# Optimization experiments

Measured on AMD Instinct MI355X. Metric: run time of the kernel, lower is better.

Reference implementation:

```python
import jax, jax.numpy as jnp
import numpy as np

N = 100000      # num nodes
E = 1600000     # num edges (avg degree 16)
IN = 128        # input_dim
D = 32          # output_dim per head
H = 4           # heads
ALPHA = 0.2     # LeakyReLU slope


def setup_inputs() -> dict:
    key = jax.random.key(0)
    k1, k2, k3, k4, k5 = jax.random.split(key, 5)
    X = jax.random.normal(k1, (N, IN), dtype=jnp.float32)
    # fc weights, xavier-like scale (bias=False in the module)
    W0 = jax.random.normal(k2, (H * D, IN), dtype=jnp.float32) * (1.0 / np.sqrt(IN))
    W1 = jax.random.normal(k3, (H * D, IN), dtype=jnp.float32) * (1.0 / np.sqrt(IN))
    a0 = jax.random.normal(k4, (H, 1, D), dtype=jnp.float32) * (1.0 / np.sqrt(D))
    deg = E // N
    # CSR rows expanded to sorted segment ids: every node has exactly `deg` out-edges
    edge_src = jnp.repeat(jnp.arange(N, dtype=jnp.int32), deg)
    column_index = jax.random.randint(k5, (E,), 0, N, dtype=jnp.int32)
    return {"X": X, "W0": W0, "W1": W1, "a0": a0,
            "edge_src": edge_src, "column_index": column_index}


def _leaky_relu(x):
    return jnp.where(x > 0, x, ALPHA * x)


def reference(X, W0, W1, a0, edge_src, column_index):
    # Linear projections, split per head: [H, N, D]
    X0 = _leaky_relu(X @ W0.T).reshape(N, H, D).transpose(1, 0, 2)
    X1 = _leaky_relu(X @ W1.T).reshape(N, H, D).transpose(1, 0, 2)
    a = a0[:, 0, :]                                    # [H, D]
    # SDDMM: att[h,e] = a[h] . (X0[h,src(e)] + X1[h,dst(e)])
    s0 = jnp.einsum('hnd,hd->hn', X0, a)               # [H, N]
    s1 = jnp.einsum('hnd,hd->hn', X1, a)
    att = s0[:, edge_src] + s1[:, column_index]        # [H, E]
    # per-head global min-max normalization, then exp (module's softmax surrogate)
    mx = jnp.max(att, axis=1, keepdims=True)
    mn = jnp.min(att, axis=1, keepdims=True)
    att = jnp.exp((att - mn) / (mx - mn))
    # sparse row-sum (softmax denominator): [N, H]
    rows_sum = jax.ops.segment_sum(att.T, edge_src, num_segments=N)
    # SpMM: aggregate neighbor features weighted by att -> [N, H, D]
    msg = att.T[:, :, None] * X1[:, column_index, :].transpose(1, 0, 2)  # [E, H, D]
    h_prime = jax.ops.segment_sum(msg, edge_src, num_segments=N)
    return h_prime / rows_sum[:, :, None]
```

## Files before the change

### kernel.cpp

```cpp
#include <hip/hip_runtime.h>
#include <hip/hip_bf16.h>

#define NN 100000
#define EE 1600000
#define ALPHA 0.2f
#define MM_BLOCKS 1563

typedef __bf16 bf16_t;
typedef __bf16 bf16x8 __attribute__((ext_vector_type(8)));
typedef __bf16 bf16x4 __attribute__((ext_vector_type(4)));
typedef float fx4 __attribute__((ext_vector_type(4)));


__global__ __launch_bounds__(512) void gemm_kernel(
    const float* __restrict__ X, const float* __restrict__ W0,
    const float* __restrict__ W1, const float* __restrict__ a0,
    bf16_t* __restrict__ F1, float* __restrict__ s0g, float* __restrict__ s1g)
{
  __shared__ uint4 lw[4096];
  const int tid  = threadIdx.x;
  const int wv   = tid >> 6;
  const int lane = tid & 63;
  const int col  = lane & 15;
  const int quad = lane >> 4;

#pragma unroll
  for (int i = 0; i < 8; ++i) {
    const int task = i * 512 + tid;
    const int sct = task >> 8, sks = (task >> 6) & 3, sl = task & 63;
    const int r  = sct * 16 + (sl & 15);
    const int c0 = (sks * 4 + (sl >> 4)) * 8;
    const float* src = (r < 128 ? W0 + (size_t)r * 128 : W1 + (size_t)(r - 128) * 128) + c0;
    const fx4 wa = *(const fx4*)src;
    const fx4 wb_ = *(const fx4*)(src + 4);
    bf16x8 wf;
    wf[0] = (bf16_t)wa[0]; wf[1] = (bf16_t)wa[1];
    wf[2] = (bf16_t)wa[2]; wf[3] = (bf16_t)wa[3];
    wf[4] = (bf16_t)wb_[0]; wf[5] = (bf16_t)wb_[1];
    wf[6] = (bf16_t)wb_[2]; wf[7] = (bf16_t)wb_[3];
    lw[task] = __builtin_bit_cast(uint4, wf);
  }
  __syncthreads();

  const int tile = blockIdx.x * 8 + wv;
  if (tile >= (NN / 16)) return;
  const int n0   = tile * 16;
  const int node = n0 + col;

  fx4 acc[16];
#pragma unroll
  for (int c = 0; c < 16; ++c) {
    acc[c][0] = 0.f; acc[c][1] = 0.f; acc[c][2] = 0.f; acc[c][3] = 0.f;
  }

  const float* xrow = X + (size_t)node * 128 + quad * 8;
#pragma unroll
  for (int ks = 0; ks < 4; ++ks) {
    fx4 xa = *(const fx4*)(xrow + ks * 32);
    fx4 xb = *(const fx4*)(xrow + ks * 32 + 4);
    bf16x8 xf;
    xf[0] = (bf16_t)xa[0]; xf[1] = (bf16_t)xa[1];
    xf[2] = (bf16_t)xa[2]; xf[3] = (bf16_t)xa[3];
    xf[4] = (bf16_t)xb[0]; xf[5] = (bf16_t)xb[1];
    xf[6] = (bf16_t)xb[2]; xf[7] = (bf16_t)xb[3];
#pragma unroll
    for (int ct = 0; ct < 16; ++ct) {
      const uint4 w4 = lw[(ct * 4 + ks) * 64 + lane];
      const bf16x8 wf = __builtin_bit_cast(bf16x8, w4);
      acc[ct] = __builtin_amdgcn_mfma_f32_16x16x32_bf16(wf, xf, acc[ct], 0, 0, 0);
    }
  }

  float sdot[8];
#pragma unroll
  for (int s = 0; s < 8; ++s) sdot[s] = 0.f;

#pragma unroll
  for (int ct = 0; ct < 16; ++ct) {
    const fx4 av = *(const fx4*)(a0 + (ct & 7) * 16 + quad * 4);
#pragma unroll
    for (int r = 0; r < 4; ++r) {
      float v = acc[ct][r];
      v = v > 0.f ? v : ALPHA * v;
      acc[ct][r] = v;
      sdot[ct >> 1] += v * av[r];
    }
    if (ct >= 8) {
      bf16x4 p;
      p[0] = (bf16_t)acc[ct][0]; p[1] = (bf16_t)acc[ct][1];
      p[2] = (bf16_t)acc[ct][2]; p[3] = (bf16_t)acc[ct][3];
      *(bf16x4*)(F1 + (size_t)node * 128 + (ct - 8) * 16 + quad * 4) = p;
    }
  }

#pragma unroll
  for (int s = 0; s < 8; ++s) {
    sdot[s] += __shfl_xor(sdot[s], 16);
    sdot[s] += __shfl_xor(sdot[s], 32);
  }
  if (quad == 0) {
    fx4 r0, r1;
    r0[0] = sdot[0]; r0[1] = sdot[1]; r0[2] = sdot[2]; r0[3] = sdot[3];
    r1[0] = sdot[4]; r1[1] = sdot[5]; r1[2] = sdot[6]; r1[3] = sdot[7];
    *(fx4*)(s0g + (size_t)node * 4) = r0;
    *(fx4*)(s1g + (size_t)node * 4) = r1;
  }
}

__global__ __launch_bounds__(256) void minmax1_kernel(
    const int* __restrict__ cidx, const float* __restrict__ s0g,
    const float* __restrict__ s1g, float* __restrict__ partial)
{
  __shared__ float s_red[4][8];
  const int t = blockIdx.x * 256 + threadIdx.x;
  fx4 mx, mn;
#pragma unroll
  for (int h = 0; h < 4; ++h) { mx[h] = -1e30f; mn[h] = 1e30f; }
  if (t < EE / 4) {
    const int node = t >> 2;
    const fx4 s0v = *(const fx4*)(s0g + (size_t)node * 4);
    const int4 c4 = ((const int4*)cidx)[t];
    const int cc[4] = {c4.x, c4.y, c4.z, c4.w};
#pragma unroll
    for (int j = 0; j < 4; ++j) {
      const fx4 s1v = *(const fx4*)(s1g + (size_t)cc[j] * 4);
#pragma unroll
      for (int h = 0; h < 4; ++h) {
        const float att = s0v[h] + s1v[h];
        mx[h] = fmaxf(mx[h], att);
        mn[h] = fminf(mn[h], att);
      }
    }
  }
#pragma unroll
  for (int off = 1; off < 64; off <<= 1) {
#pragma unroll
    for (int h = 0; h < 4; ++h) {
      mx[h] = fmaxf(mx[h], __shfl_xor(mx[h], off));
      mn[h] = fminf(mn[h], __shfl_xor(mn[h], off));
    }
  }
  const int wv = threadIdx.x >> 6;
  if ((threadIdx.x & 63) == 0) {
#pragma unroll
    for (int h = 0; h < 4; ++h) {
      s_red[wv][h] = mx[h];
      s_red[wv][4 + h] = mn[h];
    }
  }
  __syncthreads();
  if (threadIdx.x < 8) {
    const int s = threadIdx.x;
    float v = s_red[0][s];
    if (s < 4) { v = fmaxf(v, s_red[1][s]); v = fmaxf(v, s_red[2][s]); v = fmaxf(v, s_red[3][s]); }
    else       { v = fminf(v, s_red[1][s]); v = fminf(v, s_red[2][s]); v = fminf(v, s_red[3][s]); }
    partial[blockIdx.x * 8 + s] = v;
  }
}

__global__ __launch_bounds__(256) void minmax2_kernel(
    const float* __restrict__ partial, float* __restrict__ mm)
{
  __shared__ float s_red[4][8];
  fx4 mx, mn;
#pragma unroll
  for (int h = 0; h < 4; ++h) { mx[h] = -1e30f; mn[h] = 1e30f; }
  for (int g = threadIdx.x; g < MM_BLOCKS; g += 256) {
    const fx4 p0 = *(const fx4*)(partial + g * 8);
    const fx4 p1 = *(const fx4*)(partial + g * 8 + 4);
#pragma unroll
    for (int h = 0; h < 4; ++h) {
      mx[h] = fmaxf(mx[h], p0[h]);
      mn[h] = fminf(mn[h], p1[h]);
    }
  }
#pragma unroll
  for (int off = 1; off < 64; off <<= 1) {
#pragma unroll
    for (int h = 0; h < 4; ++h) {
      mx[h] = fmaxf(mx[h], __shfl_xor(mx[h], off));
      mn[h] = fminf(mn[h], __shfl_xor(mn[h], off));
    }
  }
  const int wv = threadIdx.x >> 6;
  if ((threadIdx.x & 63) == 0) {
#pragma unroll
    for (int h = 0; h < 4; ++h) {
      s_red[wv][h] = mx[h];
      s_red[wv][4 + h] = mn[h];
    }
  }
  __syncthreads();
  if (threadIdx.x < 8) {
    const int s = threadIdx.x;
    float v = s_red[0][s];
    if (s < 4) { v = fmaxf(v, s_red[1][s]); v = fmaxf(v, s_red[2][s]); v = fmaxf(v, s_red[3][s]); }
    else       { v = fminf(v, s_red[1][s]); v = fminf(v, s_red[2][s]); v = fminf(v, s_red[3][s]); }
    mm[s] = v;
  }
}

__global__ __launch_bounds__(256) void aggregate_kernel(
    const int* __restrict__ cidx, const float* __restrict__ s0g,
    const float* __restrict__ s1g, const bf16_t* __restrict__ F1,
    const float* __restrict__ mm, float* __restrict__ out)
{
  const int t = blockIdx.x * 256 + threadIdx.x;
  const int node = t >> 4;
  if (node >= NN) return;
  const int sub = t & 15;
  const int h = sub >> 2;
  const float mxv = mm[h];
  const float mnv = mm[4 + h];
  const float scale = 1.f / (mxv - mnv);
  const float s0v = s0g[node * 4 + h];
  float a_[8] = {0.f, 0.f, 0.f, 0.f, 0.f, 0.f, 0.f, 0.f};
  float wsum = 0.f;
  const int4* ce4 = (const int4*)(cidx + (size_t)node * 16);
#pragma unroll
  for (int q = 0; q < 4; ++q) {
    const int4 c4 = ce4[q];
    const int cc[4] = {c4.x, c4.y, c4.z, c4.w};
#pragma unroll
    for (int j = 0; j < 4; ++j) {
      const int c = cc[j];
      const float att = s0v + s1g[c * 4 + h];
      const float w = __expf((att - mnv) * scale);
      bf16x8 f = *(const bf16x8*)(F1 + (size_t)c * 128 + sub * 8);
#pragma unroll
      for (int k = 0; k < 8; ++k) a_[k] += w * (float)f[k];
      wsum += w;
    }
  }
  const float inv = 1.f / wsum;
  fx4 r0, r1;
#pragma unroll
  for (int j = 0; j < 4; ++j) { r0[j] = a_[j] * inv; r1[j] = a_[4 + j] * inv; }
  float* op = out + (size_t)node * 128 + sub * 8;
  *(fx4*)op = r0;
  *(fx4*)(op + 4) = r1;
}

extern "C" void kernel_launch(void* const* d_in, const int* in_sizes, int n_in,
                              void* d_out, int out_size, void* d_ws, size_t ws_size,
                              hipStream_t stream)
{
  const float* X   = (const float*)d_in[0];
  const float* W0  = (const float*)d_in[1];
  const float* W1  = (const float*)d_in[2];
  const float* a0  = (const float*)d_in[3];
  const int* cidx  = (const int*)d_in[5];
  char* ws = (char*)d_ws;
  bf16_t*   F1      = (bf16_t*)(ws + 65536);
  float*    s0g     = (float*)(ws + 25665536);
  float*    s1g     = (float*)(ws + 27265536);
  float*    mm      = (float*)(ws + 28865536);
  float*    partial = (float*)(ws + 28865600);
  float*    out     = (float*)d_out;

  gemm_kernel<<<782, 512, 0, stream>>>(X, W0, W1, a0, F1, s0g, s1g);
  minmax1_kernel<<<MM_BLOCKS, 256, 0, stream>>>(cidx, s0g, s1g, partial);
  minmax2_kernel<<<1, 256, 0, stream>>>(partial, mm);
  aggregate_kernel<<<6250, 256, 0, stream>>>(cidx, s0g, s1g, F1, mm, out);
}
```

Baseline: 212.8 us.

## Pre-convert weights once, DMA them into LDS, and batch gathers in aggregation

A small kernel now converts W0/W1 to the bf16 MFMA-tiled layout once per call. The GEMM blocks load that table straight into LDS with global_load_lds, so each of the 782 blocks no longer repeats the fp32 loads and conversions. The aggregation loop is restructured to issue eight neighbor gathers (s1 scores and F1 rows) before consuming them, which raises memory-level parallelism. The cost is one extra kernel launch, plus more registers in the aggregation kernel that may lower occupancy.

Measured after the change: 207.2 us. -2.7%, faster.

```diff
diff --git a/kernel.cpp b/kernel.cpp
--- a/kernel.cpp
+++ b/kernel.cpp
@@ -1,5 +1,6 @@
 #include <hip/hip_runtime.h>
 #include <hip/hip_bf16.h>
+#include <stdint.h>
 
 #define NN 100000
 #define EE 1600000
@@ -12,9 +13,29 @@
 typedef float fx4 __attribute__((ext_vector_type(4)));
 
 
+__global__ __launch_bounds__(512) void wconv_kernel(
+    const float* __restrict__ W0, const float* __restrict__ W1,
+    uint4* __restrict__ Wtab)
+{
+  const int task = blockIdx.x * 512 + threadIdx.x;
+  if (task >= 4096) return;
+  const int sct = task >> 8, sks = (task >> 6) & 3, sl = task & 63;
+  const int r  = sct * 16 + (sl & 15);
+  const int c0 = (sks * 4 + (sl >> 4)) * 8;
+  const float* src = (r < 128 ? W0 + (size_t)r * 128 : W1 + (size_t)(r - 128) * 128) + c0;
+  const fx4 wa = *(const fx4*)src;
+  const fx4 wb = *(const fx4*)(src + 4);
+  bf16x8 wf;
+  wf[0] = (bf16_t)wa[0]; wf[1] = (bf16_t)wa[1];
+  wf[2] = (bf16_t)wa[2]; wf[3] = (bf16_t)wa[3];
+  wf[4] = (bf16_t)wb[0]; wf[5] = (bf16_t)wb[1];
+  wf[6] = (bf16_t)wb[2]; wf[7] = (bf16_t)wb[3];
+  Wtab[task] = __builtin_bit_cast(uint4, wf);
+}
+
 __global__ __launch_bounds__(512) void gemm_kernel(
-    const float* __restrict__ X, const float* __restrict__ W0,
-    const float* __restrict__ W1, const float* __restrict__ a0,
+    const float* __restrict__ X, const uint4* __restrict__ Wtab,
+    const float* __restrict__ a0,
     bf16_t* __restrict__ F1, float* __restrict__ s0g, float* __restrict__ s1g)
 {
   __shared__ uint4 lw[4096];
@@ -27,18 +48,9 @@
 #pragma unroll
   for (int i = 0; i < 8; ++i) {
     const int task = i * 512 + tid;
-    const int sct = task >> 8, sks = (task >> 6) & 3, sl = task & 63;
-    const int r  = sct * 16 + (sl & 15);
-    const int c0 = (sks * 4 + (sl >> 4)) * 8;
-    const float* src = (r < 128 ? W0 + (size_t)r * 128 : W1 + (size_t)(r - 128) * 128) + c0;
-    const fx4 wa = *(const fx4*)src;
-    const fx4 wb_ = *(const fx4*)(src + 4);
-    bf16x8 wf;
-    wf[0] = (bf16_t)wa[0]; wf[1] = (bf16_t)wa[1];
-    wf[2] = (bf16_t)wa[2]; wf[3] = (bf16_t)wa[3];
-    wf[4] = (bf16_t)wb_[0]; wf[5] = (bf16_t)wb_[1];
-    wf[6] = (bf16_t)wb_[2]; wf[7] = (bf16_t)wb_[3];
-    lw[task] = __builtin_bit_cast(uint4, wf);
+    __builtin_amdgcn_global_load_lds(
+        (const __attribute__((address_space(1))) uint32_t*)(Wtab + task),
+        (__attribute__((address_space(3))) uint32_t*)(&lw[task]), 16, 0, 0);
   }
   __syncthreads();
 
@@ -216,22 +228,31 @@
   const float s0v = s0g[node * 4 + h];
   float a_[8] = {0.f, 0.f, 0.f, 0.f, 0.f, 0.f, 0.f, 0.f};
   float wsum = 0.f;
+
   const int4* ce4 = (const int4*)(cidx + (size_t)node * 16);
-#pragma unroll
-  for (int q = 0; q < 4; ++q) {
-    const int4 c4 = ce4[q];
-    const int cc[4] = {c4.x, c4.y, c4.z, c4.w};
-#pragma unroll
-    for (int j = 0; j < 4; ++j) {
-      const int c = cc[j];
-      const float att = s0v + s1g[c * 4 + h];
-      const float w = __expf((att - mnv) * scale);
-      bf16x8 f = *(const bf16x8*)(F1 + (size_t)c * 128 + sub * 8);
-#pragma unroll
-      for (int k = 0; k < 8; ++k) a_[k] += w * (float)f[k];
+  const int4 c01 = ce4[0], c23 = ce4[1], c45 = ce4[2], c67 = ce4[3];
+  const int cc[16] = {c01.x, c01.y, c01.z, c01.w, c23.x, c23.y, c23.z, c23.w,
+                      c45.x, c45.y, c45.z, c45.w, c67.x, c67.y, c67.z, c67.w};
+
+#pragma unroll
+  for (int half = 0; half < 2; ++half) {
+    float s1v[8];
+    bf16x8 f[8];
+#pragma unroll
+    for (int j = 0; j < 8; ++j) {
+      const int c = cc[half * 8 + j];
+      s1v[j] = s1g[(size_t)c * 4 + h];
+      f[j] = *(const bf16x8*)(F1 + (size_t)c * 128 + sub * 8);
+    }
+#pragma unroll
+    for (int j = 0; j < 8; ++j) {
+      const float w = __expf((s0v + s1v[j] - mnv) * scale);
       wsum += w;
-    }
-  }
+#pragma unroll
+      for (int k = 0; k < 8; ++k) a_[k] += w * (float)f[j][k];
+    }
+  }
+
   const float inv = 1.f / wsum;
   fx4 r0, r1;
 #pragma unroll
@@ -251,6 +272,7 @@
   const float* a0  = (const float*)d_in[3];
   const int* cidx  = (const int*)d_in[5];
   char* ws = (char*)d_ws;
+  uint4*    Wtab    = (uint4*)ws;
   bf16_t*   F1      = (bf16_t*)(ws + 65536);
   float*    s0g     = (float*)(ws + 25665536);
   float*    s1g     = (float*)(ws + 27265536);
@@ -258,7 +280,8 @@
   float*    partial = (float*)(ws + 28865600);
   float*    out     = (float*)d_out;
 
-  gemm_kernel<<<782, 512, 0, stream>>>(X, W0, W1, a0, F1, s0g, s1g);
+  wconv_kernel<<<8, 512, 0, stream>>>(W0, W1, Wtab);
+  gemm_kernel<<<782, 512, 0, stream>>>(X, Wtab, a0, F1, s0g, s1g);
   minmax1_kernel<<<MM_BLOCKS, 256, 0, stream>>>(cidx, s0g, s1g, partial);
   minmax2_kernel<<<1, 256, 0, stream>>>(partial, mm);
   aggregate_kernel<<<6250, 256, 0, stream>>>(cidx, s0g, s1g, F1, mm, out);
```
